# Kernel tuning notes

Hardware: AMD Instinct MI355X
Metric: run time of the kernel (lower is better)

The kernel has to match this reference:

```python
import jax, jax.numpy as jnp
from jax import lax
import numpy as np

NUM_LAYERS, HIDDEN, INPUT, OUT = 6, 256, 128, 10
B, T = 128, 512


def setup_inputs() -> dict:
    key = jax.random.key(0)
    ks = jax.random.split(key, 9)
    s = 0.05  # keep gate pre-activations in a sane range
    return {
        "x": jax.random.normal(ks[0], (B, T, INPUT), jnp.float32),
        "h0": jax.random.normal(ks[1], (NUM_LAYERS, B, HIDDEN), jnp.float32) * s,
        "c0": jax.random.normal(ks[2], (NUM_LAYERS, B, HIDDEN), jnp.float32) * s,
        "w_ih": jax.random.normal(ks[3], (NUM_LAYERS, 4 * HIDDEN, HIDDEN), jnp.float32) * s,
        "w_hh": jax.random.normal(ks[4], (NUM_LAYERS, 4 * HIDDEN, HIDDEN), jnp.float32) * s,
        "b_ih": jax.random.normal(ks[5], (NUM_LAYERS, 4 * HIDDEN), jnp.float32) * s,
        "b_hh": jax.random.normal(ks[6], (NUM_LAYERS, 4 * HIDDEN), jnp.float32) * s,
        "fc_w": jax.random.normal(ks[7], (OUT, HIDDEN), jnp.float32) * s,
        "fc_b": jax.random.normal(ks[8], (OUT,), jnp.float32) * s,
    }


def _lstm_layer(xseq, h, c, wih, whh, bih, bhh):
    # xseq: [B,T,D]; precompute input-to-gate GEMM for the whole sequence.
    gx = jnp.einsum("btd,gd->btg", xseq, wih) + (bih + bhh)  # [B,T,4H]

    def step(carry, g_t):
        h, c = carry
        g = g_t + h @ whh.T  # [B,4H], PyTorch gate order i,f,g,o
        i, f, gg, o = jnp.split(g, 4, axis=-1)
        c = jax.nn.sigmoid(f) * c + jax.nn.sigmoid(i) * jnp.tanh(gg)
        h = jax.nn.sigmoid(o) * jnp.tanh(c)
        return (h, c), h

    (_, _), hs = lax.scan(step, (h, c), jnp.swapaxes(gx, 0, 1))  # hs: [T,B,H]
    return jnp.swapaxes(hs, 0, 1)  # [B,T,H]


def reference(x, h0, c0, w_ih, w_hh, b_ih, b_hh, fc_w, fc_b):
    # Zero-pad input features 128 -> 256 so the packed [4H,256] layer-0 w_ih
    # applies identically to using its first 128 columns.
    seq = jnp.pad(x, ((0, 0), (0, 0), (0, HIDDEN - INPUT)))
    for l in range(NUM_LAYERS):
        seq = _lstm_layer(seq, h0[l], c0[l], w_ih[l], w_hh[l], b_ih[l], b_hh[l])
    return seq[:, -1, :] @ fc_w.T + fc_b  # [B,OUT]
```

## Files before the change

kernel.cpp:

```cpp
#include <hip/hip_runtime.h>
#include <stdint.h>

#define NLAYER 6
#define BATCH  128
#define HID    256
#define TSEQ   512
#define INFEAT 128
#define DEPTH  8
#define OUTN   10

typedef __attribute__((ext_vector_type(8))) short bf16x8;
typedef __attribute__((ext_vector_type(4))) float f32x4;

__device__ __forceinline__ short f2bf(float f) {
  union { float f; uint32_t u; } v; v.f = f;
  uint32_t r = v.u + 0x7fffu + ((v.u >> 16) & 1u);
  return (short)(r >> 16);
}
__device__ __forceinline__ float bf2f(uint32_t b) {
  union { uint32_t u; float f; } v; v.u = b << 16;
  return v.f;
}
__device__ __forceinline__ bf16x8 cvt8(const float* p) {
  f32x4 a = *(const f32x4*)p;
  f32x4 b = *(const f32x4*)(p + 4);
  bf16x8 r;
  r[0] = f2bf(a[0]); r[1] = f2bf(a[1]); r[2] = f2bf(a[2]); r[3] = f2bf(a[3]);
  r[4] = f2bf(b[0]); r[5] = f2bf(b[1]); r[6] = f2bf(b[2]); r[7] = f2bf(b[3]);
  return r;
}
__device__ __forceinline__ float sigm(float x)  { return 1.0f / (1.0f + __expf(-x)); }
__device__ __forceinline__ float tanhff(float x){ return 1.0f - 2.0f / (__expf(2.0f * x) + 1.0f); }

__device__ __forceinline__ bf16x8 load_frag_dc(const uint16_t* p) {
  union { unsigned long long q[2]; bf16x8 v; } u;
  u.q[0] = __hip_atomic_load((const unsigned long long*)p,
                             __ATOMIC_RELAXED, __HIP_MEMORY_SCOPE_AGENT);
  u.q[1] = __hip_atomic_load((const unsigned long long*)(p + 4),
                             __ATOMIC_RELAXED, __HIP_MEMORY_SCOPE_AGENT);
  return u.v;
}
__device__ __forceinline__ void store_u16_dc(uint16_t* p, uint16_t v) {
  __hip_atomic_store(p, v, __ATOMIC_RELAXED, __HIP_MEMORY_SCOPE_AGENT);
}
__device__ __forceinline__ bool flags_full(const uint16_t* f) {
  unsigned long long a = __hip_atomic_load((const unsigned long long*)f,
                                           __ATOMIC_RELAXED, __HIP_MEMORY_SCOPE_AGENT);
  unsigned long long b = __hip_atomic_load((const unsigned long long*)(f + 4),
                                           __ATOMIC_RELAXED, __HIP_MEMORY_SCOPE_AGENT);
  return (a & b) == 0x0001000100010001ULL;
}

__global__ void __launch_bounds__(256, 1)
lstm_pipeline(const float* __restrict__ xin, const float* __restrict__ h0,
              const float* __restrict__ c0,  const float* __restrict__ wih,
              const float* __restrict__ whh, const float* __restrict__ bih,
              const float* __restrict__ bhh, const float* __restrict__ fcw,
              const float* __restrict__ fcb, float* __restrict__ out,
              uint16_t* flags, uint16_t* hbuf)
{
  const int bid  = blockIdx.x;
  const int xcd  = bid & 7;
  const int slot = bid >> 3;
  const int grp  = (slot >> 3) * 8 + xcd;
  const int cg   = slot & 7;
  const int l  = grp >> 2;
  const int bs = grp & 3;

  const int tid  = threadIdx.x;
  const int wv   = tid >> 6, lane = tid & 63;
  const int wm   = wv & 1,  wu   = wv >> 1;
  const int l15  = lane & 15, l4 = lane >> 4;

  bf16x8 wf[2][4][8];
  float  bias[4];
  {
    const float* Wl[2] = { wih + (size_t)l * 1024 * 256,
                           whh + (size_t)l * 1024 * 256 };
#pragma unroll
    for (int mat = 0; mat < 2; ++mat) {
#pragma unroll
      for (int gt = 0; gt < 4; ++gt) {
        const int Rg = gt * 256 + cg * 32 + wu * 16 + l15;
        const float* rp = Wl[mat] + (size_t)Rg * 256 + l4 * 8;
#pragma unroll
        for (int kk = 0; kk < 8; ++kk)
          wf[mat][gt][kk] = cvt8(rp + kk * 32);
      }
    }
#pragma unroll
    for (int gt = 0; gt < 4; ++gt) {
      const int Rg = gt * 256 + cg * 32 + wu * 16 + l15;
      bias[gt] = bih[l * 1024 + Rg] + bhh[l * 1024 + Rg];
    }
  }

  const int ucol  = cg * 32 + wu * 16 + l15;
  const int mrowA = bs * 32 + wm * 16 + l15;
  const int mrow0 = bs * 32 + wm * 16 + l4*4;

  float c[4];
#pragma unroll
  for (int j = 0; j < 4; ++j)
    c[j] = c0[((size_t)l * BATCH + (mrow0 + j)) * HID + ucol];

  uint16_t*       fOwn = flags + ((size_t)grp * TSEQ) * 8;
  const uint16_t* fX   = (l > 0) ? flags + ((size_t)((l - 1) * 4 + bs) * TSEQ) * 8 : nullptr;
  const uint16_t* fC   = (l < 5) ? flags + ((size_t)((l + 1) * 4 + bs) * TSEQ) * 8 : nullptr;

  const uint16_t* hbL = hbuf + (size_t)l * DEPTH * BATCH * HID;
  const uint16_t* hbX = (l > 0) ? hbuf + (size_t)(l - 1) * DEPTH * BATCH * HID : nullptr;
  uint16_t*       hbO = hbuf + (size_t)l * DEPTH * BATCH * HID;

  for (int t = 0; t < TSEQ; ++t) {
    f32x4 acc[4];
#pragma unroll
    for (int gt = 0; gt < 4; ++gt) { f32x4 a = {bias[gt], bias[gt], bias[gt], bias[gt]}; acc[gt] = a; }

    if (l == 0) {
      const float* xp = xin + ((size_t)mrowA * TSEQ + t) * INFEAT + l4 * 8;
#pragma unroll
      for (int kk = 0; kk < 4; ++kk) {
        bf16x8 af = cvt8(xp + kk * 32);
#pragma unroll
        for (int gt = 0; gt < 4; ++gt)
          acc[gt] = __builtin_amdgcn_mfma_f32_16x16x32_bf16(af, wf[0][gt][kk], acc[gt], 0, 0, 0);
      }
    } else {
      const uint16_t* fx = fX + (size_t)t * 8;
      while (!flags_full(fx)) { }
      const uint16_t* hp = hbX + ((size_t)(t & (DEPTH - 1)) * BATCH + mrowA) * HID + l4 * 8;
#pragma unroll
      for (int kk = 0; kk < 8; ++kk) {
        bf16x8 af = load_frag_dc(hp + kk * 32);
#pragma unroll
        for (int gt = 0; gt < 4; ++gt)
          acc[gt] = __builtin_amdgcn_mfma_f32_16x16x32_bf16(af, wf[0][gt][kk], acc[gt], 0, 0, 0);
      }
    }

    if (t == 0) {
      const float* hp = h0 + ((size_t)l * BATCH + mrowA) * HID + l4 * 8;
#pragma unroll
      for (int kk = 0; kk < 8; ++kk) {
        bf16x8 af = cvt8(hp + kk * 8 * 4);
#pragma unroll
        for (int gt = 0; gt < 4; ++gt)
          acc[gt] = __builtin_amdgcn_mfma_f32_16x16x32_bf16(af, wf[1][gt][kk], acc[gt], 0, 0, 0);
      }
    } else {
      const uint16_t* fp = fOwn + (size_t)(t - 1) * 8;
      while (!flags_full(fp)) { }
      const uint16_t* hp = hbL + ((size_t)((t - 1) & (DEPTH - 1)) * BATCH + mrowA) * HID + l4 * 8;
#pragma unroll
      for (int kk = 0; kk < 8; ++kk) {
        bf16x8 af = load_frag_dc(hp + kk * 32);
#pragma unroll
        for (int gt = 0; gt < 4; ++gt)
          acc[gt] = __builtin_amdgcn_mfma_f32_16x16x32_bf16(af, wf[1][gt][kk], acc[gt], 0, 0, 0);
      }
    }

    if (l < 5 && t >= DEPTH) {
      const uint16_t* fc = fC + (size_t)(t - DEPTH) * 8;
      while (!flags_full(fc)) __builtin_amdgcn_s_sleep(2);
    }

    uint16_t* op = hbO + (size_t)(t & (DEPTH - 1)) * BATCH * HID;
#pragma unroll
    for (int j = 0; j < 4; ++j) {
      float iv = sigm(acc[0][j]);
      float fv = sigm(acc[1][j]);
      float gv = tanhff(acc[2][j]);
      float ov = sigm(acc[3][j]);
      float cc = fv * c[j] + iv * gv;
      c[j] = cc;
      float hv = ov * tanhff(cc);
      store_u16_dc(op + (size_t)(mrow0 + j) * HID + ucol, (uint16_t)f2bf(hv));
    }
    __syncthreads();
    if (tid == 0)
      store_u16_dc(&fOwn[(size_t)t * 8 + cg], (uint16_t)1);
  }

  if (l == 5 && cg == 0) {
    const uint16_t* fl = fOwn + (size_t)(TSEQ - 1) * 8;
    while (!flags_full(fl)) __builtin_amdgcn_s_sleep(1);
    const uint16_t* hp = hbL + (size_t)((TSEQ - 1) & (DEPTH - 1)) * BATCH * HID;
    for (int p = tid; p < 32 * OUTN; p += 256) {
      const int mr = bs * 32 + p / OUTN, oc = p % OUTN;
      float a = fcb[oc];
      const uint16_t* hr = hp + (size_t)mr * HID;
      const float* wr = fcw + oc * HID;
#pragma unroll
      for (int uu = 0; uu < HID; uu += 4) {
        unsigned long long q = __hip_atomic_load((const unsigned long long*)(hr + uu),
                                                 __ATOMIC_RELAXED, __HIP_MEMORY_SCOPE_AGENT);
        a += bf2f((uint32_t)(q & 0xffff))        * wr[uu]
           + bf2f((uint32_t)((q >> 16) & 0xffff)) * wr[uu + 1]
           + bf2f((uint32_t)((q >> 32) & 0xffff)) * wr[uu + 2]
           + bf2f((uint32_t)(q >> 48))            * wr[uu + 3];
      }
      out[mr * OUTN + oc] = a;
    }
  }
}

extern "C" void kernel_launch(void* const* d_in, const int* in_sizes, int n_in,
                              void* d_out, int out_size, void* d_ws, size_t ws_size,
                              hipStream_t stream) {
  const float* xin = (const float*)d_in[0];
  const float* h0  = (const float*)d_in[1];
  const float* c0  = (const float*)d_in[2];
  const float* wih = (const float*)d_in[3];
  const float* whh = (const float*)d_in[4];
  const float* bih = (const float*)d_in[5];
  const float* bhh = (const float*)d_in[6];
  const float* fcw = (const float*)d_in[7];
  const float* fcb = (const float*)d_in[8];
  float* out = (float*)d_out;

  uint16_t* flags = (uint16_t*)d_ws;
  const size_t flagBytes = (size_t)24 * TSEQ * 8 * sizeof(uint16_t);
  uint16_t* hbuf = (uint16_t*)((char*)d_ws + 0x40000);

  hipMemsetAsync(d_ws, 0, flagBytes, stream);
  lstm_pipeline<<<dim3(192), dim3(256), 0, stream>>>(
      xin, h0, c0, wih, whh, bih, bhh, fcw, fcb, out, flags, hbuf);
}
```

Before: 3.341 ms.

## Split K dimension across two wave halves with LDS reduction and per-wave flags

Doubles the block to 512 threads and splits the 256-wide K reduction into two halves, so each wave does half the MFMAs and holds half the weight registers. Partial sums from the second half go through double-buffered shared memory and are reduced by the first half, which then applies the gate nonlinearities. Synchronisation moves to per-wave byte flags (32 per record), and both input and recurrent flags are polled together before any loads instead of one after the other. This shortens the serial per-step critical path at the cost of an extra __syncthreads and an LDS round trip each timestep.

```diff
diff --git a/kernel.cpp b/kernel.cpp
--- a/kernel.cpp
+++ b/kernel.cpp
@@ -43,21 +43,28 @@
 __device__ __forceinline__ void store_u16_dc(uint16_t* p, uint16_t v) {
   __hip_atomic_store(p, v, __ATOMIC_RELAXED, __HIP_MEMORY_SCOPE_AGENT);
 }
-__device__ __forceinline__ bool flags_full(const uint16_t* f) {
+__device__ __forceinline__ void store_u8_dc(uint8_t* p, uint8_t v) {
+  __hip_atomic_store(p, v, __ATOMIC_RELAXED, __HIP_MEMORY_SCOPE_AGENT);
+}
+__device__ __forceinline__ bool rec_full(const uint8_t* f) {
   unsigned long long a = __hip_atomic_load((const unsigned long long*)f,
                                            __ATOMIC_RELAXED, __HIP_MEMORY_SCOPE_AGENT);
-  unsigned long long b = __hip_atomic_load((const unsigned long long*)(f + 4),
-                                           __ATOMIC_RELAXED, __HIP_MEMORY_SCOPE_AGENT);
-  return (a & b) == 0x0001000100010001ULL;
-}
-
-__global__ void __launch_bounds__(256, 1)
+  unsigned long long b = __hip_atomic_load((const unsigned long long*)(f + 8),
+                                           __ATOMIC_RELAXED, __HIP_MEMORY_SCOPE_AGENT);
+  unsigned long long c = __hip_atomic_load((const unsigned long long*)(f + 16),
+                                           __ATOMIC_RELAXED, __HIP_MEMORY_SCOPE_AGENT);
+  unsigned long long d = __hip_atomic_load((const unsigned long long*)(f + 24),
+                                           __ATOMIC_RELAXED, __HIP_MEMORY_SCOPE_AGENT);
+  return ((a & b & c & d) == 0x0101010101010101ULL);
+}
+
+__global__ void __launch_bounds__(512, 2)
 lstm_pipeline(const float* __restrict__ xin, const float* __restrict__ h0,
               const float* __restrict__ c0,  const float* __restrict__ wih,
               const float* __restrict__ whh, const float* __restrict__ bih,
               const float* __restrict__ bhh, const float* __restrict__ fcw,
               const float* __restrict__ fcb, float* __restrict__ out,
-              uint16_t* flags, uint16_t* hbuf)
+              uint8_t* flags, uint16_t* hbuf)
 {
   const int bid  = blockIdx.x;
   const int xcd  = bid & 7;
@@ -69,11 +76,13 @@
 
   const int tid  = threadIdx.x;
   const int wv   = tid >> 6, lane = tid & 63;
-  const int wm   = wv & 1,  wu   = wv >> 1;
+  const int wm   = wv & 1;
+  const int wu   = (wv >> 1) & 1;
+  const int ks   = wv >> 2;
   const int l15  = lane & 15, l4 = lane >> 4;
 
-  bf16x8 wf[2][4][8];
-  float  bias[4];
+  bf16x8 wf[2][4][4];
+  float  bias[4] = {0.f, 0.f, 0.f, 0.f};
   {
     const float* Wl[2] = { wih + (size_t)l * 1024 * 256,
                            whh + (size_t)l * 1024 * 256 };
@@ -82,16 +91,18 @@
 #pragma unroll
       for (int gt = 0; gt < 4; ++gt) {
         const int Rg = gt * 256 + cg * 32 + wu * 16 + l15;
-        const float* rp = Wl[mat] + (size_t)Rg * 256 + l4 * 8;
-#pragma unroll
-        for (int kk = 0; kk < 8; ++kk)
-          wf[mat][gt][kk] = cvt8(rp + kk * 32);
-      }
-    }
-#pragma unroll
-    for (int gt = 0; gt < 4; ++gt) {
-      const int Rg = gt * 256 + cg * 32 + wu * 16 + l15;
-      bias[gt] = bih[l * 1024 + Rg] + bhh[l * 1024 + Rg];
+        const float* rp = Wl[mat] + (size_t)Rg * 256 + ks * 128 + l4 * 8;
+#pragma unroll
+        for (int kk4 = 0; kk4 < 4; ++kk4)
+          wf[mat][gt][kk4] = cvt8(rp + kk4 * 32);
+      }
+    }
+    if (ks == 0) {
+#pragma unroll
+      for (int gt = 0; gt < 4; ++gt) {
+        const int Rg = gt * 256 + cg * 32 + wu * 16 + l15;
+        bias[gt] = bih[l * 1024 + Rg] + bhh[l * 1024 + Rg];
+      }
     }
   }
 
@@ -99,95 +110,126 @@
   const int mrowA = bs * 32 + wm * 16 + l15;
   const int mrow0 = bs * 32 + wm * 16 + l4*4;
 
-  float c[4];
-#pragma unroll
-  for (int j = 0; j < 4; ++j)
-    c[j] = c0[((size_t)l * BATCH + (mrow0 + j)) * HID + ucol];
-
-  uint16_t*       fOwn = flags + ((size_t)grp * TSEQ) * 8;
-  const uint16_t* fX   = (l > 0) ? flags + ((size_t)((l - 1) * 4 + bs) * TSEQ) * 8 : nullptr;
-  const uint16_t* fC   = (l < 5) ? flags + ((size_t)((l + 1) * 4 + bs) * TSEQ) * 8 : nullptr;
+  float c[4] = {0.f, 0.f, 0.f, 0.f};
+  if (ks == 0) {
+#pragma unroll
+    for (int j = 0; j < 4; ++j)
+      c[j] = c0[((size_t)l * BATCH + (mrow0 + j)) * HID + ucol];
+  }
+
+  const uint8_t* fXr = (l > 0) ? flags + ((size_t)((l - 1) * 4 + bs) * TSEQ) * 32 : nullptr;
+  uint8_t*       fOr = flags + ((size_t)grp * TSEQ) * 32;
+  const uint8_t* fCr = (l < 5) ? flags + ((size_t)((l + 1) * 4 + bs) * TSEQ) * 32 : nullptr;
 
   const uint16_t* hbL = hbuf + (size_t)l * DEPTH * BATCH * HID;
   const uint16_t* hbX = (l > 0) ? hbuf + (size_t)(l - 1) * DEPTH * BATCH * HID : nullptr;
   uint16_t*       hbO = hbuf + (size_t)l * DEPTH * BATCH * HID;
 
+  __shared__ f32x4 lred[2][4][4][64];
+
   for (int t = 0; t < TSEQ; ++t) {
+    {
+      bool needx = (l > 0), needh = (t > 0);
+      const uint8_t* fx = needx ? fXr + (size_t)t * 32 : nullptr;
+      const uint8_t* fo = needh ? fOr + (size_t)(t - 1) * 32 : nullptr;
+      while (needx || needh) {
+        if (needx && rec_full(fx)) needx = false;
+        if (needh && rec_full(fo)) needh = false;
+      }
+    }
+
     f32x4 acc[4];
 #pragma unroll
-    for (int gt = 0; gt < 4; ++gt) { f32x4 a = {bias[gt], bias[gt], bias[gt], bias[gt]}; acc[gt] = a; }
+    for (int gt = 0; gt < 4; ++gt) {
+      f32x4 a = {bias[gt], bias[gt], bias[gt], bias[gt]};
+      acc[gt] = a;
+    }
+
+    bf16x8 ah[4];
+    if (t == 0) {
+      const float* hp = h0 + ((size_t)l * BATCH + mrowA) * HID + ks * 128 + l4 * 8;
+#pragma unroll
+      for (int kk4 = 0; kk4 < 4; ++kk4) ah[kk4] = cvt8(hp + kk4 * 32);
+    } else {
+      const uint16_t* hp = hbL + ((size_t)((t - 1) & (DEPTH - 1)) * BATCH + mrowA) * HID
+                         + ks * 128 + l4 * 8;
+#pragma unroll
+      for (int kk4 = 0; kk4 < 4; ++kk4) ah[kk4] = load_frag_dc(hp + kk4 * 32);
+    }
 
     if (l == 0) {
-      const float* xp = xin + ((size_t)mrowA * TSEQ + t) * INFEAT + l4 * 8;
-#pragma unroll
-      for (int kk = 0; kk < 4; ++kk) {
-        bf16x8 af = cvt8(xp + kk * 32);
+      if (ks == 0) {
+        const float* xp = xin + ((size_t)mrowA * TSEQ + t) * INFEAT + l4 * 8;
+        bf16x8 ax[4];
+#pragma unroll
+        for (int kk4 = 0; kk4 < 4; ++kk4) ax[kk4] = cvt8(xp + kk4 * 32);
+#pragma unroll
+        for (int kk4 = 0; kk4 < 4; ++kk4)
+#pragma unroll
+          for (int gt = 0; gt < 4; ++gt)
+            acc[gt] = __builtin_amdgcn_mfma_f32_16x16x32_bf16(ax[kk4], wf[0][gt][kk4], acc[gt], 0, 0, 0);
+      }
+    } else {
+      const uint16_t* hp = hbX + ((size_t)(t & (DEPTH - 1)) * BATCH + mrowA) * HID
+                         + ks * 128 + l4 * 8;
+      bf16x8 ax[4];
+#pragma unroll
+      for (int kk4 = 0; kk4 < 4; ++kk4) ax[kk4] = load_frag_dc(hp + kk4 * 32);
+#pragma unroll
+      for (int kk4 = 0; kk4 < 4; ++kk4)
 #pragma unroll
         for (int gt = 0; gt < 4; ++gt)
-          acc[gt] = __builtin_amdgcn_mfma_f32_16x16x32_bf16(af, wf[0][gt][kk], acc[gt], 0, 0, 0);
-      }
-    } else {
-      const uint16_t* fx = fX + (size_t)t * 8;
-      while (!flags_full(fx)) { }
-      const uint16_t* hp = hbX + ((size_t)(t & (DEPTH - 1)) * BATCH + mrowA) * HID + l4 * 8;
-#pragma unroll
-      for (int kk = 0; kk < 8; ++kk) {
-        bf16x8 af = load_frag_dc(hp + kk * 32);
-#pragma unroll
-        for (int gt = 0; gt < 4; ++gt)
-          acc[gt] = __builtin_amdgcn_mfma_f32_16x16x32_bf16(af, wf[0][gt][kk], acc[gt], 0, 0, 0);
-      }
-    }
-
-    if (t == 0) {
-      const float* hp = h0 + ((size_t)l * BATCH + mrowA) * HID + l4 * 8;
-#pragma unroll
-      for (int kk = 0; kk < 8; ++kk) {
-        bf16x8 af = cvt8(hp + kk * 8 * 4);
-#pragma unroll
-        for (int gt = 0; gt < 4; ++gt)
-          acc[gt] = __builtin_amdgcn_mfma_f32_16x16x32_bf16(af, wf[1][gt][kk], acc[gt], 0, 0, 0);
-      }
-    } else {
-      const uint16_t* fp = fOwn + (size_t)(t - 1) * 8;
-      while (!flags_full(fp)) { }
-      const uint16_t* hp = hbL + ((size_t)((t - 1) & (DEPTH - 1)) * BATCH + mrowA) * HID + l4 * 8;
-#pragma unroll
-      for (int kk = 0; kk < 8; ++kk) {
-        bf16x8 af = load_frag_dc(hp + kk * 32);
-#pragma unroll
-        for (int gt = 0; gt < 4; ++gt)
-          acc[gt] = __builtin_amdgcn_mfma_f32_16x16x32_bf16(af, wf[1][gt][kk], acc[gt], 0, 0, 0);
-      }
-    }
-
-    if (l < 5 && t >= DEPTH) {
-      const uint16_t* fc = fC + (size_t)(t - DEPTH) * 8;
-      while (!flags_full(fc)) __builtin_amdgcn_s_sleep(2);
-    }
-
-    uint16_t* op = hbO + (size_t)(t & (DEPTH - 1)) * BATCH * HID;
-#pragma unroll
-    for (int j = 0; j < 4; ++j) {
-      float iv = sigm(acc[0][j]);
-      float fv = sigm(acc[1][j]);
-      float gv = tanhff(acc[2][j]);
-      float ov = sigm(acc[3][j]);
-      float cc = fv * c[j] + iv * gv;
-      c[j] = cc;
-      float hv = ov * tanhff(cc);
-      store_u16_dc(op + (size_t)(mrow0 + j) * HID + ucol, (uint16_t)f2bf(hv));
+          acc[gt] = __builtin_amdgcn_mfma_f32_16x16x32_bf16(ax[kk4], wf[0][gt][kk4], acc[gt], 0, 0, 0);
+    }
+
+#pragma unroll
+    for (int kk4 = 0; kk4 < 4; ++kk4)
+#pragma unroll
+      for (int gt = 0; gt < 4; ++gt)
+        acc[gt] = __builtin_amdgcn_mfma_f32_16x16x32_bf16(ah[kk4], wf[1][gt][kk4], acc[gt], 0, 0, 0);
+
+    if (ks == 1) {
+#pragma unroll
+      for (int gt = 0; gt < 4; ++gt)
+        lred[t & 1][wm * 2 + wu][gt][lane] = acc[gt];
     }
     __syncthreads();
-    if (tid == 0)
-      store_u16_dc(&fOwn[(size_t)t * 8 + cg], (uint16_t)1);
+
+    if (ks == 0) {
+#pragma unroll
+      for (int gt = 0; gt < 4; ++gt) {
+        f32x4 p = lred[t & 1][wm * 2 + wu][gt][lane];
+        acc[gt][0] += p[0]; acc[gt][1] += p[1]; acc[gt][2] += p[2]; acc[gt][3] += p[3];
+      }
+
+      if (l < 5 && t >= DEPTH) {
+        const uint8_t* fc = fCr + (size_t)(t - DEPTH) * 32;
+        while (!rec_full(fc)) __builtin_amdgcn_s_sleep(2);
+      }
+
+      uint16_t* op = hbO + (size_t)(t & (DEPTH - 1)) * BATCH * HID;
+#pragma unroll
+      for (int j = 0; j < 4; ++j) {
+        float iv = sigm(acc[0][j]);
+        float fv = sigm(acc[1][j]);
+        float gv = tanhff(acc[2][j]);
+        float ov = sigm(acc[3][j]);
+        float cc = fv * c[j] + iv * gv;
+        c[j] = cc;
+        float hv = ov * tanhff(cc);
+        store_u16_dc(op + (size_t)(mrow0 + j) * HID + ucol, (uint16_t)f2bf(hv));
+      }
+      asm volatile("s_waitcnt vmcnt(0)" ::: "memory");
+      if (lane == 0)
+        store_u8_dc(fOr + (size_t)t * 32 + (cg * 4 + wm * 2 + wu), (uint8_t)1);
+    }
   }
 
   if (l == 5 && cg == 0) {
-    const uint16_t* fl = fOwn + (size_t)(TSEQ - 1) * 8;
-    while (!flags_full(fl)) __builtin_amdgcn_s_sleep(1);
+    const uint8_t* fl = fOr + (size_t)(TSEQ - 1) * 32;
+    while (!rec_full(fl)) __builtin_amdgcn_s_sleep(1);
     const uint16_t* hp = hbL + (size_t)((TSEQ - 1) & (DEPTH - 1)) * BATCH * HID;
-    for (int p = tid; p < 32 * OUTN; p += 256) {
+    for (int p = tid; p < 32 * OUTN; p += 512) {
       const int mr = bs * 32 + p / OUTN, oc = p % OUTN;
       float a = fcb[oc];
       const uint16_t* hr = hp + (size_t)mr * HID;
@@ -196,7 +238,7 @@
       for (int uu = 0; uu < HID; uu += 4) {
         unsigned long long q = __hip_atomic_load((const unsigned long long*)(hr + uu),
                                                  __ATOMIC_RELAXED, __HIP_MEMORY_SCOPE_AGENT);
-        a += bf2f((uint32_t)(q & 0xffff))        * wr[uu]
+        a += bf2f((uint32_t)(q & 0xffff))         * wr[uu]
            + bf2f((uint32_t)((q >> 16) & 0xffff)) * wr[uu + 1]
            + bf2f((uint32_t)((q >> 32) & 0xffff)) * wr[uu + 2]
            + bf2f((uint32_t)(q >> 48))            * wr[uu + 3];
@@ -220,11 +262,11 @@
   const float* fcb = (const float*)d_in[8];
   float* out = (float*)d_out;
 
-  uint16_t* flags = (uint16_t*)d_ws;
-  const size_t flagBytes = (size_t)24 * TSEQ * 8 * sizeof(uint16_t);
-  uint16_t* hbuf = (uint16_t*)((char*)d_ws + 0x40000);
+  uint8_t* flags = (uint8_t*)d_ws;
+  const size_t flagBytes = (size_t)24 * TSEQ * 32;
+  uint16_t* hbuf = (uint16_t*)((char*)d_ws + 0x80000);
 
   hipMemsetAsync(d_ws, 0, flagBytes, stream);
-  lstm_pipeline<<<dim3(192), dim3(256), 0, stream>>>(
+  lstm_pipeline<<<dim3(192), dim3(512), 0, stream>>>(
       xin, h0, c0, wih, whh, bih, bhh, fcw, fcb, out, flags, hbuf);
 }
```

Result: slower. 4.393 ms (+31.5%).

## Use per-wave flags instead of block barrier, move input weights to LDS

Applied to the files above, without the earlier changes.

Replaces the per-block __syncthreads plus single-thread flag store with a per-wave byte flag written after a vmcnt wait, so consumers wait only on the half of the batch rows they read rather than the whole block. The input-to-hidden weights move from registers into LDS, which frees VGPRs, and both dependency waits are hoisted and polled together before the loads. The goal is lower step-to-step latency in the wavefront pipeline, paid for by extra LDS reads per step and more flag polling traffic.

```diff
diff --git a/kernel.cpp b/kernel.cpp
--- a/kernel.cpp
+++ b/kernel.cpp
@@ -43,12 +43,15 @@
 __device__ __forceinline__ void store_u16_dc(uint16_t* p, uint16_t v) {
   __hip_atomic_store(p, v, __ATOMIC_RELAXED, __HIP_MEMORY_SCOPE_AGENT);
 }
-__device__ __forceinline__ bool flags_full(const uint16_t* f) {
+__device__ __forceinline__ void store_u8_dc(uint8_t* p, uint8_t v) {
+  __hip_atomic_store(p, v, __ATOMIC_RELAXED, __HIP_MEMORY_SCOPE_AGENT);
+}
+__device__ __forceinline__ bool rec_half(const uint8_t* f) {
   unsigned long long a = __hip_atomic_load((const unsigned long long*)f,
                                            __ATOMIC_RELAXED, __HIP_MEMORY_SCOPE_AGENT);
-  unsigned long long b = __hip_atomic_load((const unsigned long long*)(f + 4),
+  unsigned long long b = __hip_atomic_load((const unsigned long long*)(f + 8),
                                            __ATOMIC_RELAXED, __HIP_MEMORY_SCOPE_AGENT);
-  return (a & b) == 0x0001000100010001ULL;
+  return ((a & b) == 0x0101010101010101ULL);
 }
 
 __global__ void __launch_bounds__(256, 1)
@@ -57,7 +60,7 @@
               const float* __restrict__ whh, const float* __restrict__ bih,
               const float* __restrict__ bhh, const float* __restrict__ fcw,
               const float* __restrict__ fcb, float* __restrict__ out,
-              uint16_t* flags, uint16_t* hbuf)
+              uint8_t* flags, uint16_t* hbuf)
 {
   const int bid  = blockIdx.x;
   const int xcd  = bid & 7;
@@ -72,28 +75,34 @@
   const int wm   = wv & 1,  wu   = wv >> 1;
   const int l15  = lane & 15, l4 = lane >> 4;
 
-  bf16x8 wf[2][4][8];
+  __shared__ bf16x8 lds_wih[4096];
+  {
+    const float* W = wih + (size_t)l * 1024 * 256;
+    for (int lin = tid; lin < 4096; lin += 256) {
+      const int l4s = lin & 3;
+      const int u5  = (lin >> 2) & 31;
+      const int kk  = (lin >> 7) & 7;
+      const int gt  = lin >> 10;
+      const int row = gt * 256 + cg * 32 + u5;
+      lds_wih[lin] = cvt8(W + (size_t)row * 256 + kk * 32 + l4s * 8);
+    }
+  }
+
+  bf16x8 wh[4][8];
   float  bias[4];
   {
-    const float* Wl[2] = { wih + (size_t)l * 1024 * 256,
-                           whh + (size_t)l * 1024 * 256 };
-#pragma unroll
-    for (int mat = 0; mat < 2; ++mat) {
-#pragma unroll
-      for (int gt = 0; gt < 4; ++gt) {
-        const int Rg = gt * 256 + cg * 32 + wu * 16 + l15;
-        const float* rp = Wl[mat] + (size_t)Rg * 256 + l4 * 8;
-#pragma unroll
-        for (int kk = 0; kk < 8; ++kk)
-          wf[mat][gt][kk] = cvt8(rp + kk * 32);
-      }
-    }
+    const float* W = whh + (size_t)l * 1024 * 256;
 #pragma unroll
     for (int gt = 0; gt < 4; ++gt) {
       const int Rg = gt * 256 + cg * 32 + wu * 16 + l15;
+      const float* rp = W + (size_t)Rg * 256 + l4 * 8;
+#pragma unroll
+      for (int kk = 0; kk < 8; ++kk)
+        wh[gt][kk] = cvt8(rp + kk * 32);
       bias[gt] = bih[l * 1024 + Rg] + bhh[l * 1024 + Rg];
     }
   }
+  __syncthreads();
 
   const int ucol  = cg * 32 + wu * 16 + l15;
   const int mrowA = bs * 32 + wm * 16 + l15;
@@ -104,66 +113,81 @@
   for (int j = 0; j < 4; ++j)
     c[j] = c0[((size_t)l * BATCH + (mrow0 + j)) * HID + ucol];
 
-  uint16_t*       fOwn = flags + ((size_t)grp * TSEQ) * 8;
-  const uint16_t* fX   = (l > 0) ? flags + ((size_t)((l - 1) * 4 + bs) * TSEQ) * 8 : nullptr;
-  const uint16_t* fC   = (l < 5) ? flags + ((size_t)((l + 1) * 4 + bs) * TSEQ) * 8 : nullptr;
+  const uint8_t* fXr = (l > 0) ? flags + ((size_t)((l - 1) * 4 + bs) * TSEQ) * 32 : nullptr;
+  uint8_t*       fOr = flags + ((size_t)grp * TSEQ) * 32;
+  const uint8_t* fCr = (l < 5) ? flags + ((size_t)((l + 1) * 4 + bs) * TSEQ) * 32 : nullptr;
 
   const uint16_t* hbL = hbuf + (size_t)l * DEPTH * BATCH * HID;
   const uint16_t* hbX = (l > 0) ? hbuf + (size_t)(l - 1) * DEPTH * BATCH * HID : nullptr;
   uint16_t*       hbO = hbuf + (size_t)l * DEPTH * BATCH * HID;
 
+  const int fidx = wm * 16 + cg * 2 + wu;
+
   for (int t = 0; t < TSEQ; ++t) {
+    {
+      bool needx = (l > 0), needh = (t > 0);
+      const uint8_t* fx = needx ? fXr + (size_t)t * 32 + wm * 16 : nullptr;
+      const uint8_t* fo = needh ? fOr + (size_t)(t - 1) * 32 + wm * 16 : nullptr;
+      while (needx || needh) {
+        if (needx && rec_half(fx)) needx = false;
+        if (needh && rec_half(fo)) needh = false;
+      }
+    }
+
+    bf16x8 ah[8];
+    if (t == 0) {
+      const float* hp = h0 + ((size_t)l * BATCH + mrowA) * HID + l4 * 8;
+#pragma unroll
+      for (int kk = 0; kk < 8; ++kk) ah[kk] = cvt8(hp + kk * 32);
+    } else {
+      const uint16_t* hp = hbL + ((size_t)((t - 1) & (DEPTH - 1)) * BATCH + mrowA) * HID + l4 * 8;
+#pragma unroll
+      for (int kk = 0; kk < 8; ++kk) ah[kk] = load_frag_dc(hp + kk * 32);
+    }
+
     f32x4 acc[4];
 #pragma unroll
-    for (int gt = 0; gt < 4; ++gt) { f32x4 a = {bias[gt], bias[gt], bias[gt], bias[gt]}; acc[gt] = a; }
-
+    for (int gt = 0; gt < 4; ++gt) {
+      f32x4 a = {bias[gt], bias[gt], bias[gt], bias[gt]};
+      acc[gt] = a;
+    }
+
+    const int bbase = (wu * 16 + l15) * 4 + l4;
     if (l == 0) {
       const float* xp = xin + ((size_t)mrowA * TSEQ + t) * INFEAT + l4 * 8;
 #pragma unroll
       for (int kk = 0; kk < 4; ++kk) {
-        bf16x8 af = cvt8(xp + kk * 32);
-#pragma unroll
-        for (int gt = 0; gt < 4; ++gt)
-          acc[gt] = __builtin_amdgcn_mfma_f32_16x16x32_bf16(af, wf[0][gt][kk], acc[gt], 0, 0, 0);
+        bf16x8 axr = cvt8(xp + kk * 32);
+#pragma unroll
+        for (int gt = 0; gt < 4; ++gt) {
+          bf16x8 b = lds_wih[gt * 1024 + kk * 128 + bbase];
+          acc[gt] = __builtin_amdgcn_mfma_f32_16x16x32_bf16(axr, b, acc[gt], 0, 0, 0);
+        }
       }
     } else {
-      const uint16_t* fx = fX + (size_t)t * 8;
-      while (!flags_full(fx)) { }
+      bf16x8 ax[8];
       const uint16_t* hp = hbX + ((size_t)(t & (DEPTH - 1)) * BATCH + mrowA) * HID + l4 * 8;
 #pragma unroll
+      for (int kk = 0; kk < 8; ++kk) ax[kk] = load_frag_dc(hp + kk * 32);
+#pragma unroll
       for (int kk = 0; kk < 8; ++kk) {
-        bf16x8 af = load_frag_dc(hp + kk * 32);
-#pragma unroll
-        for (int gt = 0; gt < 4; ++gt)
-          acc[gt] = __builtin_amdgcn_mfma_f32_16x16x32_bf16(af, wf[0][gt][kk], acc[gt], 0, 0, 0);
-      }
-    }
-
-    if (t == 0) {
-      const float* hp = h0 + ((size_t)l * BATCH + mrowA) * HID + l4 * 8;
-#pragma unroll
-      for (int kk = 0; kk < 8; ++kk) {
-        bf16x8 af = cvt8(hp + kk * 8 * 4);
-#pragma unroll
-        for (int gt = 0; gt < 4; ++gt)
-          acc[gt] = __builtin_amdgcn_mfma_f32_16x16x32_bf16(af, wf[1][gt][kk], acc[gt], 0, 0, 0);
-      }
-    } else {
-      const uint16_t* fp = fOwn + (size_t)(t - 1) * 8;
-      while (!flags_full(fp)) { }
-      const uint16_t* hp = hbL + ((size_t)((t - 1) & (DEPTH - 1)) * BATCH + mrowA) * HID + l4 * 8;
-#pragma unroll
-      for (int kk = 0; kk < 8; ++kk) {
-        bf16x8 af = load_frag_dc(hp + kk * 32);
-#pragma unroll
-        for (int gt = 0; gt < 4; ++gt)
-          acc[gt] = __builtin_amdgcn_mfma_f32_16x16x32_bf16(af, wf[1][gt][kk], acc[gt], 0, 0, 0);
-      }
-    }
+#pragma unroll
+        for (int gt = 0; gt < 4; ++gt) {
+          bf16x8 b = lds_wih[gt * 1024 + kk * 128 + bbase];
+          acc[gt] = __builtin_amdgcn_mfma_f32_16x16x32_bf16(ax[kk], b, acc[gt], 0, 0, 0);
+        }
+      }
+    }
+
+#pragma unroll
+    for (int kk = 0; kk < 8; ++kk)
+#pragma unroll
+      for (int gt = 0; gt < 4; ++gt)
+        acc[gt] = __builtin_amdgcn_mfma_f32_16x16x32_bf16(ah[kk], wh[gt][kk], acc[gt], 0, 0, 0);
 
     if (l < 5 && t >= DEPTH) {
-      const uint16_t* fc = fC + (size_t)(t - DEPTH) * 8;
-      while (!flags_full(fc)) __builtin_amdgcn_s_sleep(2);
+      const uint8_t* fc = fCr + (size_t)(t - DEPTH) * 32 + wm * 16;
+      while (!rec_half(fc)) __builtin_amdgcn_s_sleep(2);
     }
 
     uint16_t* op = hbO + (size_t)(t & (DEPTH - 1)) * BATCH * HID;
@@ -178,14 +202,14 @@
       float hv = ov * tanhff(cc);
       store_u16_dc(op + (size_t)(mrow0 + j) * HID + ucol, (uint16_t)f2bf(hv));
     }
-    __syncthreads();
-    if (tid == 0)
-      store_u16_dc(&fOwn[(size_t)t * 8 + cg], (uint16_t)1);
+    asm volatile("s_waitcnt vmcnt(0)" ::: "memory");
+    if (lane == 0)
+      store_u8_dc(fOr + (size_t)t * 32 + fidx, (uint8_t)1);
   }
 
   if (l == 5 && cg == 0) {
-    const uint16_t* fl = fOwn + (size_t)(TSEQ - 1) * 8;
-    while (!flags_full(fl)) __builtin_amdgcn_s_sleep(1);
+    const uint8_t* fl = fOr + (size_t)(TSEQ - 1) * 32;
+    while (!(rec_half(fl) && rec_half(fl + 16))) __builtin_amdgcn_s_sleep(1);
     const uint16_t* hp = hbL + (size_t)((TSEQ - 1) & (DEPTH - 1)) * BATCH * HID;
     for (int p = tid; p < 32 * OUTN; p += 256) {
       const int mr = bs * 32 + p / OUTN, oc = p % OUTN;
@@ -196,7 +220,7 @@
       for (int uu = 0; uu < HID; uu += 4) {
         unsigned long long q = __hip_atomic_load((const unsigned long long*)(hr + uu),
                                                  __ATOMIC_RELAXED, __HIP_MEMORY_SCOPE_AGENT);
-        a += bf2f((uint32_t)(q & 0xffff))        * wr[uu]
+        a += bf2f((uint32_t)(q & 0xffff))         * wr[uu]
            + bf2f((uint32_t)((q >> 16) & 0xffff)) * wr[uu + 1]
            + bf2f((uint32_t)((q >> 32) & 0xffff)) * wr[uu + 2]
            + bf2f((uint32_t)(q >> 48))            * wr[uu + 3];
@@ -220,9 +244,9 @@
   const float* fcb = (const float*)d_in[8];
   float* out = (float*)d_out;
 
-  uint16_t* flags = (uint16_t*)d_ws;
-  const size_t flagBytes = (size_t)24 * TSEQ * 8 * sizeof(uint16_t);
-  uint16_t* hbuf = (uint16_t*)((char*)d_ws + 0x40000);
+  uint8_t* flags = (uint8_t*)d_ws;
+  const size_t flagBytes = (size_t)24 * TSEQ * 32;
+  uint16_t* hbuf = (uint16_t*)((char*)d_ws + 0x80000);
 
   hipMemsetAsync(d_ws, 0, flagBytes, stream);
   lstm_pipeline<<<dim3(192), dim3(256), 0, stream>>>(
```

Result: slower. 3.419 ms (+2.3%).
